# Optimization experiments

Measured on AMD Instinct MI355X. Metric: run time of the kernel, lower is better.

Reference implementation:

```python
import jax, jax.numpy as jnp
import numpy as np

N_NODES = 100000
N_EDGES = 1600000
IN_F = 128
HID_F = 128
OUT_F = 128
HEAD_HID = 128
HEAD_OUT = 64


def setup_inputs() -> dict:
    key = jax.random.key(0)
    ks = jax.random.split(key, 16)
    glorot = lambda k, i, o: jax.random.normal(k, (i, o), jnp.float32) * (2.0 / (i + o)) ** 0.5
    return {
        "x": jax.random.normal(ks[0], (N_NODES, IN_F), jnp.float32),
        "src": jax.random.randint(ks[1], (N_EDGES,), 0, N_NODES),
        "dst": jax.random.randint(ks[2], (N_EDGES,), 0, N_NODES),
        "eps1": jnp.zeros((), jnp.float32),
        "eps2": jnp.zeros((), jnp.float32),
        # mlp_fun1: in_feats -> hid -> hid
        "w11": glorot(ks[3], IN_F, HID_F), "b11": jnp.zeros((HID_F,), jnp.float32),
        "w12": glorot(ks[4], HID_F, HID_F), "b12": jnp.zeros((HID_F,), jnp.float32),
        # mlp_fun2: hid -> hid -> out_feats
        "w21": glorot(ks[5], HID_F, HID_F), "b21": jnp.zeros((HID_F,), jnp.float32),
        "w22": glorot(ks[6], HID_F, OUT_F), "b22": jnp.zeros((OUT_F,), jnp.float32),
        # head mlp: out_feats -> hidden_dim -> output_dim (sigmoid)
        "wm1": glorot(ks[7], OUT_F, HEAD_HID), "bm1": jnp.zeros((HEAD_HID,), jnp.float32),
        "wm2": glorot(ks[8], HEAD_HID, HEAD_OUT), "bm2": jnp.zeros((HEAD_OUT,), jnp.float32),
    }


def _mlp2(h, w1, b1, w2, b2):
    # 2-layer MLP: Linear -> ReLU -> Linear
    return jax.nn.relu(h @ w1 + b1) @ w2 + b2


def _gin_conv(x, src, dst, eps, w1, b1, w2, b2):
    # sum-aggregate over incoming edges, then MLP update (DGL GINConv, learn_eps)
    agg = jax.ops.segment_sum(x[src], dst, num_segments=x.shape[0])  # [N, d]
    return _mlp2((1.0 + eps) * x + agg, w1, b1, w2, b2)


def reference(x, src, dst, eps1, eps2, w11, b11, w12, b12,
              w21, b21, w22, b22, wm1, bm1, wm2, bm2):
    # dropout is identity in eval mode
    h = jax.nn.relu(_gin_conv(x, src, dst, eps1, w11, b11, w12, b12))
    h = jax.nn.relu(_gin_conv(h, src, dst, eps2, w21, b21, w22, b22))
    # head MLP producing per-node probabilities (consumed by log-prob loss)
    return jax.nn.sigmoid(_mlp2(h, wm1, bm1, wm2, bm2))  # [N, output_dim]
```

## Files before the change

kernel.cpp:

```cpp
#include <hip/hip_runtime.h>

static constexpr int NN = 100000;
static constexpr int NE = 1600000;
static constexpr int NBUK = (NN + 255) / 256;
static constexpr int SC_BLOCKS = 400;
static constexpr int SC_CH = NE / SC_BLOCKS;

typedef __bf16    bf16x8 __attribute__((ext_vector_type(8)));
typedef float     f32x4  __attribute__((ext_vector_type(4)));
typedef _Float16  f16x8  __attribute__((ext_vector_type(8)));

__device__ __forceinline__ unsigned short f2b(float f){
  unsigned u = __builtin_bit_cast(unsigned, f);
  u += 0x7fffu + ((u >> 16) & 1u);
  return (unsigned short)(u >> 16);
}
__device__ __forceinline__ float b2f(unsigned short b){
  return __builtin_bit_cast(float, (unsigned)b << 16);
}

__device__ __forceinline__ void split1(float v, __bf16& h, __bf16& l){
  unsigned short hb = f2b(v);
  float hf = b2f(hb);
  h = __builtin_bit_cast(__bf16, hb);
  l = __builtin_bit_cast(__bf16, f2b(v - hf));
}

__device__ __forceinline__ void split8f(const float* __restrict__ p, bf16x8& h, bf16x8& l){
  #pragma unroll
  for (int j=0;j<8;j++){
    __bf16 hh, ll; split1(p[j], hh, ll); h[j] = hh; l[j] = ll;
  }
}
__device__ __forceinline__ void split8h(f16x8 v, bf16x8& h, bf16x8& l){
  #pragma unroll
  for (int j=0;j<8;j++){
    __bf16 hh, ll; split1((float)v[j], hh, ll); h[j] = hh; l[j] = ll;
  }
}

__device__ __forceinline__ unsigned pkh(float x, float y){
  unsigned short a = __builtin_bit_cast(unsigned short, (_Float16)x);
  unsigned short b = __builtin_bit_cast(unsigned short, (_Float16)y);
  return (unsigned)a | ((unsigned)b << 16);
}
__device__ __forceinline__ float2 uph(unsigned u){
  _Float16 a = __builtin_bit_cast(_Float16, (unsigned short)(u & 0xffffu));
  _Float16 b = __builtin_bit_cast(_Float16, (unsigned short)(u >> 16));
  return make_float2((float)a, (float)b);
}

__global__ void k_pack(const float* __restrict__ w11, const float* __restrict__ w12,
                       const float* __restrict__ w21, const float* __restrict__ w22,
                       const float* __restrict__ wm1, const float* __restrict__ wm2,
                       unsigned short* __restrict__ p11h, unsigned short* __restrict__ p11l,
                       unsigned short* __restrict__ p12h, unsigned short* __restrict__ p12l,
                       unsigned short* __restrict__ p21h, unsigned short* __restrict__ p21l,
                       unsigned short* __restrict__ p22h, unsigned short* __restrict__ p22l,
                       unsigned short* __restrict__ pm1h, unsigned short* __restrict__ pm1l,
                       unsigned short* __restrict__ pm2h, unsigned short* __restrict__ pm2l){
  int b = blockIdx.x, lane = threadIdx.x;
  const float* W; unsigned short* Ph; unsigned short* Pl; int NCT, f;
  if (b < 160){
    int m = b >> 5; f = b & 31; NCT = 8;
    W  = (m==0)?w11 :(m==1)?w12 :(m==2)?w21 :(m==3)?w22 :wm1;
    Ph = (m==0)?p11h:(m==1)?p12h:(m==2)?p21h:(m==3)?p22h:pm1h;
    Pl = (m==0)?p11l:(m==1)?p12l:(m==2)?p21l:(m==3)?p22l:pm1l;
  } else { f = b - 160; NCT = 4; W = wm2; Ph = pm2h; Pl = pm2l; }
  int NC = NCT * 16;
  int kt = f / NCT, ct = f % NCT;
  int k0 = kt*32 + ((lane>>4)*8), col = ct*16 + (lane&15);
  unsigned short* dh = Ph + ((size_t)(f*64 + lane))*8;
  unsigned short* dl = Pl + ((size_t)(f*64 + lane))*8;
  #pragma unroll
  for (int j=0;j<8;j++){
    float v = W[(size_t)(k0+j)*NC + col];
    unsigned short hb = f2b(v);
    dh[j] = hb;
    dl[j] = f2b(v - b2f(hb));
  }
}

__global__ void k_cvt(const float* __restrict__ x, unsigned* __restrict__ xh, int n4){
  int i = blockIdx.x*256 + threadIdx.x;
  if (i < n4){
    float4 v = reinterpret_cast<const float4*>(x)[i];
    uint2 o; o.x = pkh(v.x, v.y); o.y = pkh(v.z, v.w);
    reinterpret_cast<uint2*>(xh)[i] = o;
  }
}

__global__ __launch_bounds__(256) void k_hist(const int* __restrict__ dst, int* __restrict__ bhist){
  __shared__ int h[NBUK];
  int blk = blockIdx.x, t = threadIdx.x;
  for (int i=t;i<NBUK;i+=256) h[i]=0;
  __syncthreads();
  int e0 = blk*SC_CH;
  for (int e=e0+t; e<e0+SC_CH; e+=256) atomicAdd(&h[((unsigned)dst[e])>>8], 1);
  __syncthreads();
  for (int i=t;i<NBUK;i+=256){ int c=h[i]; if (c) atomicAdd(&bhist[i], c); }
}

__global__ void k_boff2(const int* __restrict__ bhist, int* __restrict__ boff){
  __shared__ int s[512];
  int t = threadIdx.x;
  int v = (t < NBUK) ? bhist[t] : 0;
  s[t] = v; __syncthreads();
  for (int off=1; off<512; off<<=1){
    int u = 0; if (t>=off) u = s[t-off];
    __syncthreads(); s[t] += u; __syncthreads();
  }
  if (t < NBUK) boff[t] = s[t] - v;
}

__global__ __launch_bounds__(256) void k_scatter1(const int* __restrict__ src,
                                                  const int* __restrict__ dst,
                                                  const int* __restrict__ boff,
                                                  int* __restrict__ gbcur,
                                                  uint2* __restrict__ tmp){
  __shared__ int hc[NBUK];
  __shared__ int hb[NBUK];
  int blk = blockIdx.x, t = threadIdx.x;
  int e0 = blk * SC_CH, e1 = e0 + SC_CH;
  for (int i=t;i<NBUK;i+=256) hc[i]=0;
  __syncthreads();
  for (int e=e0+t; e<e1; e+=256) atomicAdd(&hc[((unsigned)dst[e])>>8], 1);
  __syncthreads();
  for (int i=t;i<NBUK;i+=256){ int c = hc[i]; hb[i] = c ? atomicAdd(&gbcur[i], c) : 0; }
  __syncthreads();
  for (int i=t;i<NBUK;i+=256) hc[i]=0;
  __syncthreads();
  for (int e=e0+t; e<e1; e+=256){
    int d = dst[e]; int b = ((unsigned)d)>>8;
    int pos = atomicAdd(&hc[b], 1);
    tmp[(size_t)boff[b] + hb[b] + pos] = make_uint2((unsigned)src[e], (unsigned)d);
  }
}

__global__ __launch_bounds__(256) void k_fill2(const uint2* __restrict__ tmp,
                                               const int* __restrict__ boff,
                                               const int* __restrict__ bhist,
                                               int* __restrict__ eidx,
                                               int* __restrict__ rs, int* __restrict__ deg, int N){
  __shared__ int lh[256];
  __shared__ int ls[256];
  __shared__ int lc[256];
  int b = blockIdx.x, t = threadIdx.x;
  int base = boff[b], cnt = bhist[b];
  int nb0 = b*256;
  lh[t] = 0; lc[t] = 0;
  __syncthreads();
  for (int i=t; i<cnt; i+=256) atomicAdd(&lh[(int)tmp[(size_t)base+i].y - nb0], 1);
  __syncthreads();
  int v = lh[t];
  ls[t] = v; __syncthreads();
  for (int off=1; off<256; off<<=1){
    int u = 0; if (t>=off) u = ls[t-off];
    __syncthreads(); ls[t] += u; __syncthreads();
  }
  int node = nb0 + t;
  if (node < N){ deg[node] = v; rs[node] = base + ls[t] - v; }
  __syncthreads();
  for (int i=t; i<cnt; i+=256){
    uint2 e = tmp[(size_t)base+i];
    int local = (int)e.y - nb0;
    int pos = atomicAdd(&lc[local], 1);
    eidx[base + ls[local] - lh[local] + pos] = (int)e.x;
  }
}

__global__ __launch_bounds__(256) void k_agg(const unsigned* __restrict__ inp,
                                             unsigned* __restrict__ out,
                                             const float* __restrict__ epsp,
                                             const int* __restrict__ rs, const int* __restrict__ deg,
                                             const int* __restrict__ eidx, int N){
  int gw = (blockIdx.x*256 + threadIdx.x) >> 6;
  int lane = threadIdx.x & 63;
  if (gw >= N) return;
  float sc = 1.0f + *epsp;
  float2 v = uph(inp[(size_t)gw*64 + lane]);
  float a0 = sc * v.x, a1 = sc * v.y;
  int beg = rs[gw], d = deg[gw];
  int i = 0;
  for (; i+8 <= d; i += 8){
    unsigned u[8];
    #pragma unroll
    for (int j=0;j<8;j++) u[j] = inp[(size_t)eidx[beg+i+j]*64 + lane];
    #pragma unroll
    for (int j=0;j<8;j++){ float2 f = uph(u[j]); a0 += f.x; a1 += f.y; }
  }
  for (; i < d; ++i){
    float2 u = uph(inp[(size_t)eidx[beg+i]*64 + lane]);
    a0 += u.x; a1 += u.y;
  }
  out[(size_t)gw*64 + lane] = pkh(a0, a1);
}

__device__ __forceinline__ void load_a_glob(const _Float16* __restrict__ t, int rbase,
                                            int wv, int lane, int N,
                                            bf16x8 ah[4], bf16x8 al[4]){
  int row = rbase + wv*16 + (lane & 15); if (row >= N) row = N - 1;
  const _Float16* ap = t + (size_t)row*128 + ((lane>>4)*8);
  #pragma unroll
  for (int kt=0;kt<4;kt++){
    f16x8 v = *reinterpret_cast<const f16x8*>(ap + kt*32);
    split8h(v, ah[kt], al[kt]);
  }
}
__device__ __forceinline__ void load_a_lds(const float* base, int lane,
                                           bf16x8 ah[4], bf16x8 al[4], int stride){
  int row = lane & 15, ko = (lane>>4)*8;
  #pragma unroll
  for (int kt=0;kt<4;kt++) split8f(base + row*stride + kt*32 + ko, ah[kt], al[kt]);
}

template<int NCT>
__device__ __forceinline__ void mm_stage3(const bf16x8 ah[4], const bf16x8 al[4],
                                          const unsigned short* __restrict__ wh,
                                          const unsigned short* __restrict__ wl,
                                          int lane, f32x4 acc[NCT]){
  #pragma unroll
  for (int ct=0; ct<NCT; ++ct){
    f32x4 c = {0.f,0.f,0.f,0.f};
    #pragma unroll
    for (int kt=0; kt<4; ++kt){
      int fo = ((kt*NCT + ct)*64 + lane) << 3;
      bf16x8 bh = *reinterpret_cast<const bf16x8*>(wh + fo);
      bf16x8 bl = *reinterpret_cast<const bf16x8*>(wl + fo);
      c = __builtin_amdgcn_mfma_f32_16x16x32_bf16(ah[kt], bh, c, 0, 0, 0);
      c = __builtin_amdgcn_mfma_f32_16x16x32_bf16(al[kt], bh, c, 0, 0, 0);
      c = __builtin_amdgcn_mfma_f32_16x16x32_bf16(ah[kt], bl, c, 0, 0, 0);
    }
    acc[ct] = c;
  }
}

template<int NCT>
__device__ __forceinline__ void epi_relu_lds(const f32x4 acc[NCT], const float* __restrict__ bias,
                                             float* dst, int lane, int stride){
  int r0 = (lane>>4)*4, col0 = lane & 15;
  #pragma unroll
  for (int ct=0; ct<NCT; ++ct){
    float bv = bias[ct*16 + col0];
    #pragma unroll
    for (int r=0;r<4;r++){
      float v = fmaxf(acc[ct][r] + bv, 0.f);
      dst[(r0 + r)*stride + ct*16 + col0] = v;
    }
  }
}

static constexpr int LSTR = 132;

__global__ __launch_bounds__(256) void k_mlp1(const _Float16* __restrict__ t,
    const unsigned short* __restrict__ w1h, const unsigned short* __restrict__ w1l, const float* __restrict__ b1,
    const unsigned short* __restrict__ w2h, const unsigned short* __restrict__ w2l, const float* __restrict__ b2,
    unsigned* __restrict__ h, int N){
  __shared__ float lds[64*LSTR];
  int tid = threadIdx.x, lane = tid & 63, wv = tid >> 6;
  int rbase = blockIdx.x * 64;
  bf16x8 ah[4], al[4];
  f32x4 acc[8];
  load_a_glob(t, rbase, wv, lane, N, ah, al);
  mm_stage3<8>(ah, al, w1h, w1l, lane, acc);
  epi_relu_lds<8>(acc, b1, lds + wv*16*LSTR, lane, LSTR);
  __syncthreads();
  load_a_lds(lds + wv*16*LSTR, lane, ah, al, LSTR);
  __syncthreads();
  mm_stage3<8>(ah, al, w2h, w2l, lane, acc);
  epi_relu_lds<8>(acc, b2, lds + wv*16*LSTR, lane, LSTR);
  __syncthreads();
  int nvalid = N - rbase; if (nvalid > 64) nvalid = 64;
  uint2* dv = reinterpret_cast<uint2*>(h + (size_t)rbase*64);
  for (int i=tid; i < nvalid*32; i += 256){
    int row = i >> 5, c4 = i & 31;
    const float4 f = *reinterpret_cast<const float4*>(&lds[row*LSTR + c4*4]);
    uint2 o; o.x = pkh(f.x, f.y); o.y = pkh(f.z, f.w);
    dv[i] = o;
  }
}

__global__ __launch_bounds__(256) void k_mlp2_head(const _Float16* __restrict__ t,
    const unsigned short* __restrict__ w1h, const unsigned short* __restrict__ w1l, const float* __restrict__ b1,
    const unsigned short* __restrict__ w2h, const unsigned short* __restrict__ w2l, const float* __restrict__ b2,
    const unsigned short* __restrict__ w3h, const unsigned short* __restrict__ w3l, const float* __restrict__ b3,
    const unsigned short* __restrict__ w4h, const unsigned short* __restrict__ w4l, const float* __restrict__ b4,
    float* __restrict__ out, int N){
  __shared__ float lds[64*LSTR];
  int tid = threadIdx.x, lane = tid & 63, wv = tid >> 6;
  int rbase = blockIdx.x * 64;
  bf16x8 ah[4], al[4];
  f32x4 acc[8];
  load_a_glob(t, rbase, wv, lane, N, ah, al);
  mm_stage3<8>(ah, al, w1h, w1l, lane, acc);
  epi_relu_lds<8>(acc, b1, lds + wv*16*LSTR, lane, LSTR);
  __syncthreads();
  load_a_lds(lds + wv*16*LSTR, lane, ah, al, LSTR);
  __syncthreads();
  mm_stage3<8>(ah, al, w2h, w2l, lane, acc);
  epi_relu_lds<8>(acc, b2, lds + wv*16*LSTR, lane, LSTR);
  __syncthreads();
  load_a_lds(lds + wv*16*LSTR, lane, ah, al, LSTR);
  __syncthreads();
  mm_stage3<8>(ah, al, w3h, w3l, lane, acc);
  epi_relu_lds<8>(acc, b3, lds + wv*16*LSTR, lane, LSTR);
  __syncthreads();
  load_a_lds(lds + wv*16*LSTR, lane, ah, al, LSTR);
  __syncthreads();
  f32x4 acc4[4];
  mm_stage3<4>(ah, al, w4h, w4l, lane, acc4);
  {
    float* olds = lds;
    int r0 = (lane>>4)*4, col0 = lane & 15;
    #pragma unroll
    for (int ct=0; ct<4; ++ct){
      float bv = b4[ct*16 + col0];
      #pragma unroll
      for (int r=0;r<4;r++){
        float z = acc4[ct][r] + bv;
        float s = 1.0f / (1.0f + __expf(-z));
        olds[(wv*16 + r0 + r)*68 + ct*16 + col0] = s;
      }
    }
  }
  __syncthreads();
  int nvalid = N - rbase; if (nvalid > 64) nvalid = 64;
  float4* dv = reinterpret_cast<float4*>(out + (size_t)rbase*64);
  for (int i=tid; i < nvalid*16; i += 256){
    int row = i >> 4, c4 = i & 15;
    dv[i] = *reinterpret_cast<const float4*>(&lds[row*68 + c4*4]);
  }
}

extern "C" void kernel_launch(void* const* d_in, const int* in_sizes, int n_in,
                              void* d_out, int out_size, void* d_ws, size_t ws_size,
                              hipStream_t stream) {
  const float* x   = (const float*)d_in[0];
  const int*   src = (const int*)  d_in[1];
  const int*   dst = (const int*)  d_in[2];
  const float* eps1= (const float*)d_in[3];
  const float* eps2= (const float*)d_in[4];
  const float* w11 = (const float*)d_in[5];  const float* b11 = (const float*)d_in[6];
  const float* w12 = (const float*)d_in[7];  const float* b12 = (const float*)d_in[8];
  const float* w21 = (const float*)d_in[9];  const float* b21 = (const float*)d_in[10];
  const float* w22 = (const float*)d_in[11]; const float* b22 = (const float*)d_in[12];
  const float* wm1 = (const float*)d_in[13]; const float* bm1 = (const float*)d_in[14];
  const float* wm2 = (const float*)d_in[15]; const float* bm2 = (const float*)d_in[16];

  char* ws = (char*)d_ws;
  size_t off = 0;
  auto alloc = [&](size_t bytes) -> void* {
    void* p = ws + off;
    off = (off + bytes + 255) & ~(size_t)255;
    return p;
  };
  unsigned* xh  = (unsigned*)alloc((size_t)NN*64*4);
  unsigned* B0  = (unsigned*)alloc((size_t)NN*64*4);
  unsigned* h1h = (unsigned*)alloc((size_t)NN*64*4);
  uint2* tmp = (uint2*)alloc((size_t)NE*8);
  int* eidx = (int*)alloc((size_t)NE*4);
  int* deg  = (int*)alloc((size_t)NN*4);
  int* rs   = (int*)alloc((size_t)NN*4);
  int* bhist= (int*)alloc((size_t)NBUK*4);
  int* boff = (int*)alloc((size_t)NBUK*4);
  int* gbcur= (int*)alloc((size_t)NBUK*4);
  unsigned short* p11h = (unsigned short*)alloc(128*128*2);
  unsigned short* p11l = (unsigned short*)alloc(128*128*2);
  unsigned short* p12h = (unsigned short*)alloc(128*128*2);
  unsigned short* p12l = (unsigned short*)alloc(128*128*2);
  unsigned short* p21h = (unsigned short*)alloc(128*128*2);
  unsigned short* p21l = (unsigned short*)alloc(128*128*2);
  unsigned short* p22h = (unsigned short*)alloc(128*128*2);
  unsigned short* p22l = (unsigned short*)alloc(128*128*2);
  unsigned short* pm1h = (unsigned short*)alloc(128*128*2);
  unsigned short* pm1l = (unsigned short*)alloc(128*128*2);
  unsigned short* pm2h = (unsigned short*)alloc(128*64*2);
  unsigned short* pm2l = (unsigned short*)alloc(128*64*2);
  if (off > ws_size) return;

  hipMemsetAsync(bhist, 0, (size_t)NBUK*4, stream);
  hipMemsetAsync(gbcur, 0, (size_t)NBUK*4, stream);

  k_pack<<<176, 64, 0, stream>>>(w11,w12,w21,w22,wm1,wm2,
                                 p11h,p11l,p12h,p12l,p21h,p21l,p22h,p22l,pm1h,pm1l,pm2h,pm2l);
  k_cvt<<<(NN*32 + 255)/256, 256, 0, stream>>>(x, xh, NN*32);
  k_hist<<<SC_BLOCKS, 256, 0, stream>>>(dst, bhist);
  k_boff2<<<1, 512, 0, stream>>>(bhist, boff);
  k_scatter1<<<SC_BLOCKS, 256, 0, stream>>>(src, dst, boff, gbcur, tmp);
  k_fill2<<<NBUK, 256, 0, stream>>>(tmp, boff, bhist, eidx, rs, deg, NN);

  k_agg<<<(NN+3)/4, 256, 0, stream>>>(xh, B0, eps1, rs, deg, eidx, NN);
  k_mlp1<<<(NN+63)/64, 256, 0, stream>>>((const _Float16*)B0, p11h, p11l, b11,
                                         p12h, p12l, b12, h1h, NN);
  k_agg<<<(NN+3)/4, 256, 0, stream>>>(h1h, B0, eps2, rs, deg, eidx, NN);
  k_mlp2_head<<<(NN+63)/64, 256, 0, stream>>>((const _Float16*)B0, p21h, p21l, b21,
                                              p22h, p22l, b22, pm1h, pm1l, bm1,
                                              pm2h, pm2l, bm2, (float*)d_out, NN);
}
```

Measured before the change: 333.8 us.

## Replace 3-pass bf16 split GEMMs with fp16 hi/scaled-lo two-pass MFMA

Weights are packed as an fp16 high part plus a scaled fp16 residual, and activations stay in fp16. Each MLP stage therefore uses two f16 MFMAs per tile instead of three bf16 MFMAs, and the per-element bf16 splitting of activations is gone. Intermediate activations are kept in per-wave fp16 LDS slices, so the block-wide barriers are removed and each wave writes out its own rows. The cost is that activations are rounded to fp16 between layers, which loses some precision compared with the near-fp32 split scheme.

```diff
diff --git a/kernel.cpp b/kernel.cpp
--- a/kernel.cpp
+++ b/kernel.cpp
@@ -6,38 +6,11 @@
 static constexpr int SC_BLOCKS = 400;
 static constexpr int SC_CH = NE / SC_BLOCKS;
 
-typedef __bf16    bf16x8 __attribute__((ext_vector_type(8)));
 typedef float     f32x4  __attribute__((ext_vector_type(4)));
 typedef _Float16  f16x8  __attribute__((ext_vector_type(8)));
 
-__device__ __forceinline__ unsigned short f2b(float f){
-  unsigned u = __builtin_bit_cast(unsigned, f);
-  u += 0x7fffu + ((u >> 16) & 1u);
-  return (unsigned short)(u >> 16);
-}
-__device__ __forceinline__ float b2f(unsigned short b){
-  return __builtin_bit_cast(float, (unsigned)b << 16);
-}
-
-__device__ __forceinline__ void split1(float v, __bf16& h, __bf16& l){
-  unsigned short hb = f2b(v);
-  float hf = b2f(hb);
-  h = __builtin_bit_cast(__bf16, hb);
-  l = __builtin_bit_cast(__bf16, f2b(v - hf));
-}
-
-__device__ __forceinline__ void split8f(const float* __restrict__ p, bf16x8& h, bf16x8& l){
-  #pragma unroll
-  for (int j=0;j<8;j++){
-    __bf16 hh, ll; split1(p[j], hh, ll); h[j] = hh; l[j] = ll;
-  }
-}
-__device__ __forceinline__ void split8h(f16x8 v, bf16x8& h, bf16x8& l){
-  #pragma unroll
-  for (int j=0;j<8;j++){
-    __bf16 hh, ll; split1((float)v[j], hh, ll); h[j] = hh; l[j] = ll;
-  }
-}
+static constexpr float LO_SCALE  = 16384.0f;
+static constexpr float LO_USCALE = 1.0f / 16384.0f;
 
 __device__ __forceinline__ unsigned pkh(float x, float y){
   unsigned short a = __builtin_bit_cast(unsigned short, (_Float16)x);
@@ -75,9 +48,10 @@
   #pragma unroll
   for (int j=0;j<8;j++){
     float v = W[(size_t)(k0+j)*NC + col];
-    unsigned short hb = f2b(v);
-    dh[j] = hb;
-    dl[j] = f2b(v - b2f(hb));
+    _Float16 h = (_Float16)v;
+    _Float16 l = (_Float16)((v - (float)h) * LO_SCALE);
+    dh[j] = __builtin_bit_cast(unsigned short, h);
+    dl[j] = __builtin_bit_cast(unsigned short, l);
   }
 }
 
@@ -197,86 +171,80 @@
 }
 
 __device__ __forceinline__ void load_a_glob(const _Float16* __restrict__ t, int rbase,
-                                            int wv, int lane, int N,
-                                            bf16x8 ah[4], bf16x8 al[4]){
+                                            int wv, int lane, int N, f16x8 a[4]){
   int row = rbase + wv*16 + (lane & 15); if (row >= N) row = N - 1;
   const _Float16* ap = t + (size_t)row*128 + ((lane>>4)*8);
   #pragma unroll
-  for (int kt=0;kt<4;kt++){
-    f16x8 v = *reinterpret_cast<const f16x8*>(ap + kt*32);
-    split8h(v, ah[kt], al[kt]);
-  }
-}
-__device__ __forceinline__ void load_a_lds(const float* base, int lane,
-                                           bf16x8 ah[4], bf16x8 al[4], int stride){
+  for (int kt=0;kt<4;kt++) a[kt] = *reinterpret_cast<const f16x8*>(ap + kt*32);
+}
+__device__ __forceinline__ void load_a_lds(const _Float16* base, int lane, f16x8 a[4], int stride){
   int row = lane & 15, ko = (lane>>4)*8;
   #pragma unroll
-  for (int kt=0;kt<4;kt++) split8f(base + row*stride + kt*32 + ko, ah[kt], al[kt]);
+  for (int kt=0;kt<4;kt++) a[kt] = *reinterpret_cast<const f16x8*>(base + row*stride + kt*32 + ko);
 }
 
 template<int NCT>
-__device__ __forceinline__ void mm_stage3(const bf16x8 ah[4], const bf16x8 al[4],
-                                          const unsigned short* __restrict__ wh,
-                                          const unsigned short* __restrict__ wl,
-                                          int lane, f32x4 acc[NCT]){
+__device__ __forceinline__ void mm2(const f16x8 a[4],
+                                    const unsigned short* __restrict__ wh,
+                                    const unsigned short* __restrict__ wl,
+                                    int lane, f32x4 acc[NCT], f32x4 acc2[NCT]){
   #pragma unroll
   for (int ct=0; ct<NCT; ++ct){
-    f32x4 c = {0.f,0.f,0.f,0.f};
+    f32x4 c  = {0.f,0.f,0.f,0.f};
+    f32x4 c2 = {0.f,0.f,0.f,0.f};
     #pragma unroll
     for (int kt=0; kt<4; ++kt){
       int fo = ((kt*NCT + ct)*64 + lane) << 3;
-      bf16x8 bh = *reinterpret_cast<const bf16x8*>(wh + fo);
-      bf16x8 bl = *reinterpret_cast<const bf16x8*>(wl + fo);
-      c = __builtin_amdgcn_mfma_f32_16x16x32_bf16(ah[kt], bh, c, 0, 0, 0);
-      c = __builtin_amdgcn_mfma_f32_16x16x32_bf16(al[kt], bh, c, 0, 0, 0);
-      c = __builtin_amdgcn_mfma_f32_16x16x32_bf16(ah[kt], bl, c, 0, 0, 0);
+      f16x8 bh = *reinterpret_cast<const f16x8*>(wh + fo);
+      f16x8 bl = *reinterpret_cast<const f16x8*>(wl + fo);
+      c  = __builtin_amdgcn_mfma_f32_16x16x32_f16(a[kt], bh, c,  0, 0, 0);
+      c2 = __builtin_amdgcn_mfma_f32_16x16x32_f16(a[kt], bl, c2, 0, 0, 0);
     }
-    acc[ct] = c;
+    acc[ct] = c; acc2[ct] = c2;
   }
 }
 
 template<int NCT>
-__device__ __forceinline__ void epi_relu_lds(const f32x4 acc[NCT], const float* __restrict__ bias,
-                                             float* dst, int lane, int stride){
+__device__ __forceinline__ void epi_relu(const f32x4 acc[NCT], const f32x4 acc2[NCT],
+                                         const float* __restrict__ bias,
+                                         _Float16* dst, int lane, int stride){
   int r0 = (lane>>4)*4, col0 = lane & 15;
   #pragma unroll
   for (int ct=0; ct<NCT; ++ct){
     float bv = bias[ct*16 + col0];
     #pragma unroll
     for (int r=0;r<4;r++){
-      float v = fmaxf(acc[ct][r] + bv, 0.f);
-      dst[(r0 + r)*stride + ct*16 + col0] = v;
+      float v = fmaxf(acc[ct][r] + acc2[ct][r]*LO_USCALE + bv, 0.f);
+      dst[(r0 + r)*stride + ct*16 + col0] = (_Float16)v;
     }
   }
 }
 
-static constexpr int LSTR = 132;
+static constexpr int HSTR = 136;
+static constexpr int WSLICE = 16*HSTR;
 
 __global__ __launch_bounds__(256) void k_mlp1(const _Float16* __restrict__ t,
     const unsigned short* __restrict__ w1h, const unsigned short* __restrict__ w1l, const float* __restrict__ b1,
     const unsigned short* __restrict__ w2h, const unsigned short* __restrict__ w2l, const float* __restrict__ b2,
     unsigned* __restrict__ h, int N){
-  __shared__ float lds[64*LSTR];
+  __shared__ _Float16 lds[4*WSLICE];
   int tid = threadIdx.x, lane = tid & 63, wv = tid >> 6;
+  _Float16* slice = lds + wv*WSLICE;
   int rbase = blockIdx.x * 64;
-  bf16x8 ah[4], al[4];
-  f32x4 acc[8];
-  load_a_glob(t, rbase, wv, lane, N, ah, al);
-  mm_stage3<8>(ah, al, w1h, w1l, lane, acc);
-  epi_relu_lds<8>(acc, b1, lds + wv*16*LSTR, lane, LSTR);
-  __syncthreads();
-  load_a_lds(lds + wv*16*LSTR, lane, ah, al, LSTR);
-  __syncthreads();
-  mm_stage3<8>(ah, al, w2h, w2l, lane, acc);
-  epi_relu_lds<8>(acc, b2, lds + wv*16*LSTR, lane, LSTR);
-  __syncthreads();
-  int nvalid = N - rbase; if (nvalid > 64) nvalid = 64;
-  uint2* dv = reinterpret_cast<uint2*>(h + (size_t)rbase*64);
-  for (int i=tid; i < nvalid*32; i += 256){
-    int row = i >> 5, c4 = i & 31;
-    const float4 f = *reinterpret_cast<const float4*>(&lds[row*LSTR + c4*4]);
-    uint2 o; o.x = pkh(f.x, f.y); o.y = pkh(f.z, f.w);
-    dv[i] = o;
+  f16x8 a[4];
+  f32x4 acc[8], acc2[8];
+  load_a_glob(t, rbase, wv, lane, N, a);
+  mm2<8>(a, w1h, w1l, lane, acc, acc2);
+  epi_relu<8>(acc, acc2, b1, slice, lane, HSTR);
+  load_a_lds(slice, lane, a, HSTR);
+  mm2<8>(a, w2h, w2l, lane, acc, acc2);
+  epi_relu<8>(acc, acc2, b2, slice, lane, HSTR);
+  int wrow0 = rbase + wv*16;
+  for (int i=lane; i < 16*32; i += 64){
+    int r = i >> 5, c = i & 31;
+    if (wrow0 + r < N)
+      reinterpret_cast<uint2*>(h)[(size_t)(wrow0 + r)*32 + c] =
+        *reinterpret_cast<const uint2*>(slice + r*HSTR + c*4);
   }
 }
 
@@ -286,49 +254,45 @@
     const unsigned short* __restrict__ w3h, const unsigned short* __restrict__ w3l, const float* __restrict__ b3,
     const unsigned short* __restrict__ w4h, const unsigned short* __restrict__ w4l, const float* __restrict__ b4,
     float* __restrict__ out, int N){
-  __shared__ float lds[64*LSTR];
+  __shared__ _Float16 lds[4*WSLICE];
   int tid = threadIdx.x, lane = tid & 63, wv = tid >> 6;
+  _Float16* slice = lds + wv*WSLICE;
   int rbase = blockIdx.x * 64;
-  bf16x8 ah[4], al[4];
-  f32x4 acc[8];
-  load_a_glob(t, rbase, wv, lane, N, ah, al);
-  mm_stage3<8>(ah, al, w1h, w1l, lane, acc);
-  epi_relu_lds<8>(acc, b1, lds + wv*16*LSTR, lane, LSTR);
-  __syncthreads();
-  load_a_lds(lds + wv*16*LSTR, lane, ah, al, LSTR);
-  __syncthreads();
-  mm_stage3<8>(ah, al, w2h, w2l, lane, acc);
-  epi_relu_lds<8>(acc, b2, lds + wv*16*LSTR, lane, LSTR);
-  __syncthreads();
-  load_a_lds(lds + wv*16*LSTR, lane, ah, al, LSTR);
-  __syncthreads();
-  mm_stage3<8>(ah, al, w3h, w3l, lane, acc);
-  epi_relu_lds<8>(acc, b3, lds + wv*16*LSTR, lane, LSTR);
-  __syncthreads();
-  load_a_lds(lds + wv*16*LSTR, lane, ah, al, LSTR);
-  __syncthreads();
-  f32x4 acc4[4];
-  mm_stage3<4>(ah, al, w4h, w4l, lane, acc4);
+  f16x8 a[4];
+  f32x4 acc[8], acc2[8];
+  load_a_glob(t, rbase, wv, lane, N, a);
+  mm2<8>(a, w1h, w1l, lane, acc, acc2);
+  epi_relu<8>(acc, acc2, b1, slice, lane, HSTR);
+  load_a_lds(slice, lane, a, HSTR);
+  mm2<8>(a, w2h, w2l, lane, acc, acc2);
+  epi_relu<8>(acc, acc2, b2, slice, lane, HSTR);
+  load_a_lds(slice, lane, a, HSTR);
+  mm2<8>(a, w3h, w3l, lane, acc, acc2);
+  epi_relu<8>(acc, acc2, b3, slice, lane, HSTR);
+  load_a_lds(slice, lane, a, HSTR);
+  f32x4 acc4[4], acc4b[4];
+  mm2<4>(a, w4h, w4l, lane, acc4, acc4b);
   {
-    float* olds = lds;
+    float* olds = reinterpret_cast<float*>(slice);
     int r0 = (lane>>4)*4, col0 = lane & 15;
     #pragma unroll
     for (int ct=0; ct<4; ++ct){
       float bv = b4[ct*16 + col0];
       #pragma unroll
       for (int r=0;r<4;r++){
-        float z = acc4[ct][r] + bv;
+        float z = acc4[ct][r] + acc4b[ct][r]*LO_USCALE + bv;
         float s = 1.0f / (1.0f + __expf(-z));
-        olds[(wv*16 + r0 + r)*68 + ct*16 + col0] = s;
+        olds[(r0 + r)*68 + ct*16 + col0] = s;
       }
     }
   }
-  __syncthreads();
-  int nvalid = N - rbase; if (nvalid > 64) nvalid = 64;
-  float4* dv = reinterpret_cast<float4*>(out + (size_t)rbase*64);
-  for (int i=tid; i < nvalid*16; i += 256){
-    int row = i >> 4, c4 = i & 15;
-    dv[i] = *reinterpret_cast<const float4*>(&lds[row*68 + c4*4]);
+  const float* olds = reinterpret_cast<const float*>(slice);
+  int wrow0 = rbase + wv*16;
+  for (int i=lane; i < 16*16; i += 64){
+    int r = i >> 4, c = i & 15;
+    if (wrow0 + r < N)
+      reinterpret_cast<float4*>(out)[(size_t)(wrow0 + r)*16 + c] =
+        *reinterpret_cast<const float4*>(olds + r*68 + c*4);
   }
 }
 
```

Result: slower. 341.2 us (+2.2%).
